# Performance work log

Measured on AMD Instinct MI355X. Metric: run time of the kernel, lower is better.

The kernel has to match this reference:

```python
import jax, jax.numpy as jnp
import numpy as np

NF4_LUT = jnp.array([-1.0, -0.6961928009986877, -0.5250730514526367, -0.39491719007492065,
                     -0.28444138169288635, -0.18477343022823334, -0.08820830285549164, 0.0,
                     0.07107656449079514, 0.14263366162776947, 0.22430233657360077,
                     0.3203405737876892, 0.4407068192958832, 0.5905631184577942,
                     0.796090841293335, 1.0], dtype=jnp.float32)

BLOCK_SIZE = 64
OUT_FEATURES = 11008
IN_FEATURES = 4096


def dequantize_nf4(packed, absmax, out_shape):
    # packed: (O, I//2) int codes 0..255; absmax: (O, num_blocks)
    higher = packed // 16
    lower = packed % 16
    unpacked = jnp.stack([lower, higher], axis=-1).reshape(out_shape)  # (O, I)
    dequant = NF4_LUT[unpacked]  # LUT gather -> fp32 (O, I)
    O, I = out_shape
    # block-wise absmax scale
    dequant = (dequant.reshape(O, I // BLOCK_SIZE, BLOCK_SIZE) * absmax[:, :, None]).reshape(O, I)
    return dequant


def setup_inputs() -> dict:
    key = jax.random.key(0)
    k1, k2, k3, k4 = jax.random.split(key, 4)
    x = jax.random.normal(k1, (4, 2048, IN_FEATURES), dtype=jnp.float32)
    weight = jax.random.randint(k2, (OUT_FEATURES, IN_FEATURES // 2), 0, 256, dtype=jnp.int32)
    absmax = jax.random.uniform(k3, (OUT_FEATURES, IN_FEATURES // BLOCK_SIZE), dtype=jnp.float32)
    bias = jax.random.normal(k4, (OUT_FEATURES,), dtype=jnp.float32)
    return {"x": x, "weight": weight, "absmax": absmax, "bias": bias}


def reference(x, weight, absmax, bias):
    w = dequantize_nf4(weight, absmax, (OUT_FEATURES, IN_FEATURES))  # (O, I)
    # F.linear: y = x @ w.T + bias
    return jnp.einsum('bsi,oi->bso', x, w) + bias
```

## Files before the change

### kernel.cpp

```cpp
#include <hip/hip_runtime.h>

#define IN_F 4096
#define OUT_F 11008

typedef __attribute__((ext_vector_type(8))) short bf16x8;
typedef __attribute__((ext_vector_type(4))) float f32x4;
typedef __attribute__((ext_vector_type(4))) unsigned short us4;
typedef __attribute__((ext_vector_type(8))) unsigned short us8;

__device__ __forceinline__ unsigned short f2bf(float f) {
  unsigned int u = __float_as_uint(f);
  u += 0x7FFFu + ((u >> 16) & 1u);
  return (unsigned short)(u >> 16);
}

__global__ __launch_bounds__(256) void prepass(const float* __restrict__ X,
                                               unsigned short* __restrict__ Xb, int n8,
                                               const int* __restrict__ Wp,
                                               const float* __restrict__ Amax,
                                               unsigned short* __restrict__ Wb, int n4,
                                               int xblk) {
  __shared__ float lutS[16];
  if (threadIdx.x < 16) {
    const float lut[16] = {-1.0f, -0.6961928009986877f, -0.5250730514526367f,
        -0.39491719007492065f, -0.28444138169288635f, -0.18477343022823334f,
        -0.08820830285549164f, 0.0f, 0.07107656449079514f, 0.14263366162776947f,
        0.22430233657360077f, 0.3203405737876892f, 0.4407068192958832f,
        0.5905631184577942f, 0.796090841293335f, 1.0f};
    lutS[threadIdx.x] = lut[threadIdx.x];
  }
  __syncthreads();
  if ((int)blockIdx.x < xblk) {
    for (int i = blockIdx.x * blockDim.x + threadIdx.x; i < n8;
         i += xblk * blockDim.x) {
      const float4 a = reinterpret_cast<const float4*>(X)[2 * i];
      const float4 b = reinterpret_cast<const float4*>(X)[2 * i + 1];
      us8 h;
      h[0] = f2bf(a.x); h[1] = f2bf(a.y); h[2] = f2bf(a.z); h[3] = f2bf(a.w);
      h[4] = f2bf(b.x); h[5] = f2bf(b.y); h[6] = f2bf(b.z); h[7] = f2bf(b.w);
      reinterpret_cast<us8*>(Xb)[i] = h;
    }
  } else {
    const int wgrid = gridDim.x - xblk;
    for (int i = (blockIdx.x - xblk) * blockDim.x + threadIdx.x; i < n4;
         i += wgrid * blockDim.x) {
      const int j = i * 4;
      const int row = j >> 11;
      const int coli = j & 2047;
      const float am = Amax[row * (IN_F / 64) + (coli >> 5)];
      const int4 pk = reinterpret_cast<const int4*>(Wp)[i];
      us8 h; int c;
      c = pk.x & 255; h[0] = f2bf(lutS[c & 15] * am); h[1] = f2bf(lutS[c >> 4] * am);
      c = pk.y & 255; h[2] = f2bf(lutS[c & 15] * am); h[3] = f2bf(lutS[c >> 4] * am);
      c = pk.z & 255; h[4] = f2bf(lutS[c & 15] * am); h[5] = f2bf(lutS[c >> 4] * am);
      c = pk.w & 255; h[6] = f2bf(lutS[c & 15] * am); h[7] = f2bf(lutS[c >> 4] * am);
      reinterpret_cast<us8*>(Wb)[i] = h;
    }
  }
}

#define MF(a, b, c) __builtin_amdgcn_mfma_f32_16x16x32_bf16(a, b, c, 0, 0, 0)
#define GLDS(src, dst) __builtin_amdgcn_global_load_lds( \
    (const __attribute__((address_space(1))) void*)(src), \
    (__attribute__((address_space(3))) void*)(dst), 16, 0, 0)
#define BAR __builtin_amdgcn_s_barrier()
#define VM2 asm volatile("s_waitcnt vmcnt(2)")
#define VM0 asm volatile("s_waitcnt vmcnt(0)")
#define P1 __builtin_amdgcn_s_setprio(1)
#define P0 __builtin_amdgcn_s_setprio(0)

__global__ __launch_bounds__(1024, 4) void gemm256w16(
    const unsigned short* __restrict__ A,
    const unsigned short* __restrict__ B,
    const float* __restrict__ Bias, float* __restrict__ Out, int M) {
  extern __shared__ unsigned short sm[];
  char* const smc = (char*)sm;

  const int tid = threadIdx.x;
  const int l = tid & 63;
  const int wid = tid >> 6;

  const int Nb = OUT_F / 256;

  const int bps = 16 * Nb;
  const int pxc = bps >> 3;
  const int i6 = (int)blockIdx.x % bps;
  const int sup = (int)blockIdx.x / bps;
  const int kk = (i6 & 7) * pxc + (i6 >> 3);
  const int m0 = (sup * 16 + (kk & 15)) * 256;
  const int n0 = (kk >> 4) * 256;

  const int wm = (wid >> 2) * 64;
  const int wn = (wid & 3) * 64;

  const int lv = (l & 15) * 64 + (((l >> 4) ^ ((l >> 1) & 3)) * 16);
  const int aLane = (wid >> 2) * 4096 + lv;
  const int bLane = 16384 + (wid & 3) * 4096 + lv;

  const int rq = tid >> 2;
  const int cs = (tid & 3) ^ ((tid >> 3) & 3);
  const unsigned short* gAs = A + (size_t)(m0 + rq) * IN_F + cs * 8;
  const unsigned short* gBs = B + (size_t)(n0 + rq) * IN_F + cs * 8;

#define SA(t, sl) GLDS(gAs + (size_t)(t) * 32, sm + (sl) * 16384 + wid * 512)
#define SB(t, sl) GLDS(gBs + (size_t)(t) * 32, sm + (sl) * 16384 + 8192 + wid * 512)

  f32x4 acc[4][4];
#pragma unroll
  for (int i = 0; i < 4; ++i)
#pragma unroll
    for (int j = 0; j < 4; ++j) acc[i][j] = {0.f, 0.f, 0.f, 0.f};

#define KT(T, SL, STG, VMW) do { \
    VMW; \
    BAR; \
    const char* Sb = smc + (SL) * 32768; \
    bf16x8 a0, a1, a2, a3, b0, b1, b2, b3; \
    a0 = *(const bf16x8*)(Sb + aLane);        a1 = *(const bf16x8*)(Sb + aLane + 1024); \
    a2 = *(const bf16x8*)(Sb + aLane + 2048); a3 = *(const bf16x8*)(Sb + aLane + 3072); \
    b0 = *(const bf16x8*)(Sb + bLane);        b1 = *(const bf16x8*)(Sb + bLane + 1024); \
    if (STG) SA((T) + 2, ((SL) + 2) % 3); \
    P1; \
    acc[0][0]=MF(a0,b0,acc[0][0]); acc[0][1]=MF(a0,b1,acc[0][1]); \
    acc[1][0]=MF(a1,b0,acc[1][0]); acc[1][1]=MF(a1,b1,acc[1][1]); \
    acc[2][0]=MF(a2,b0,acc[2][0]); acc[2][1]=MF(a2,b1,acc[2][1]); \
    acc[3][0]=MF(a3,b0,acc[3][0]); acc[3][1]=MF(a3,b1,acc[3][1]); \
    P0; \
    b2 = *(const bf16x8*)(Sb + bLane + 2048); b3 = *(const bf16x8*)(Sb + bLane + 3072); \
    if (STG) SB((T) + 2, ((SL) + 2) % 3); \
    P1; \
    acc[0][2]=MF(a0,b2,acc[0][2]); acc[0][3]=MF(a0,b3,acc[0][3]); \
    acc[1][2]=MF(a1,b2,acc[1][2]); acc[1][3]=MF(a1,b3,acc[1][3]); \
    acc[2][2]=MF(a2,b2,acc[2][2]); acc[2][3]=MF(a2,b3,acc[2][3]); \
    acc[3][2]=MF(a3,b2,acc[3][2]); acc[3][3]=MF(a3,b3,acc[3][3]); \
    P0; \
  } while (0)

  SA(0, 0); SB(0, 0); SA(1, 1); SB(1, 1);

  for (int T = 0; T < 126; T += 3) {
    KT(T, 0, (T < 124), VM2);
    KT(T + 1, 1, (T + 1 < 126), VM2);
    KT(T + 2, 2, (T + 2 < 126), VM2);
  }
  KT(126, 0, 0, VM2);
  KT(127, 1, 0, VM0);

  const int crow0 = m0 + wm + ((l >> 4) << 2);
  const int ccol0 = n0 + wn + (l & 15);
#pragma unroll
  for (int j = 0; j < 4; ++j) {
    const float bv = Bias[ccol0 + j * 16];
#pragma unroll
    for (int i = 0; i < 4; ++i)
#pragma unroll
      for (int rg = 0; rg < 4; ++rg)
        Out[(size_t)(crow0 + i * 16 + rg) * OUT_F + ccol0 + j * 16] = acc[i][j][rg] + bv;
  }
}

__global__ __launch_bounds__(256, 2) void nf4_gemm_fused(
    const float* __restrict__ X, const int* __restrict__ Wp,
    const float* __restrict__ Amax, const float* __restrict__ Bias,
    float* __restrict__ Out, int M) {
  __shared__ unsigned short As[128 * 64];
  __shared__ unsigned short Bs[128 * 64];
  __shared__ float lutS[16];

  const int t = threadIdx.x;
  const int l = t & 63;
  const int wid = t >> 6;

  if (t < 16) {
    const float lut[16] = {-1.0f, -0.6961928009986877f, -0.5250730514526367f,
        -0.39491719007492065f, -0.28444138169288635f, -0.18477343022823334f,
        -0.08820830285549164f, 0.0f, 0.07107656449079514f, 0.14263366162776947f,
        0.22430233657360077f, 0.3203405737876892f, 0.4407068192958832f,
        0.5905631184577942f, 0.796090841293335f, 1.0f};
    lutS[t] = lut[t];
  }

  const int ntile = OUT_F / 128;
  const int m0 = (blockIdx.x / ntile) * 128;
  const int n0 = (blockIdx.x % ntile) * 128;

  const int ar = t >> 4;
  const int ac4 = t & 15;
  const int br = t >> 3;
  const int bg = t & 7;
  const int wm = (wid >> 1) * 64;
  const int wn = (wid & 1) * 64;

  f32x4 acc[4][4];
#pragma unroll
  for (int i = 0; i < 4; ++i)
#pragma unroll
    for (int j = 0; j < 4; ++j) acc[i][j] = {0.f, 0.f, 0.f, 0.f};

  __syncthreads();

  for (int k0 = 0; k0 < IN_F; k0 += 64) {
#pragma unroll
    for (int p = 0; p < 8; ++p) {
      const int r = p * 16 + ar;
      const float4 v = *reinterpret_cast<const float4*>(
          X + (size_t)(m0 + r) * IN_F + k0 + ac4 * 4);
      us4 h;
      h[0] = f2bf(v.x); h[1] = f2bf(v.y); h[2] = f2bf(v.z); h[3] = f2bf(v.w);
      const int byte = r * 128 + ((ac4 * 8) ^ ((r & 7) << 4));
      *reinterpret_cast<us4*>(reinterpret_cast<char*>(As) + byte) = h;
    }
#pragma unroll
    for (int p = 0; p < 4; ++p) {
      const int r = p * 32 + br;
      const float amv = Amax[(size_t)(n0 + r) * (IN_F / 64) + (k0 >> 6)];
      const int4 pk = *reinterpret_cast<const int4*>(
          Wp + (size_t)(n0 + r) * (IN_F / 2) + (k0 >> 1) + bg * 4);
      us8 h;
      {
        int c;
        c = pk.x & 255; h[0] = f2bf(lutS[c & 15] * amv); h[1] = f2bf(lutS[c >> 4] * amv);
        c = pk.y & 255; h[2] = f2bf(lutS[c & 15] * amv); h[3] = f2bf(lutS[c >> 4] * amv);
        c = pk.z & 255; h[4] = f2bf(lutS[c & 15] * amv); h[5] = f2bf(lutS[c >> 4] * amv);
        c = pk.w & 255; h[6] = f2bf(lutS[c & 15] * amv); h[7] = f2bf(lutS[c >> 4] * amv);
      }
      const int byte = r * 128 + ((bg * 16) ^ ((r & 7) << 4));
      *reinterpret_cast<us8*>(reinterpret_cast<char*>(Bs) + byte) = h;
    }
    __syncthreads();

#pragma unroll
    for (int kkk = 0; kkk < 64; kkk += 32) {
      bf16x8 af[4], bfv[4];
      const int kb = (kkk + ((l >> 4) << 3)) * 2;
#pragma unroll
      for (int i = 0; i < 4; ++i) {
        const int row = wm + i * 16 + (l & 15);
        af[i] = *reinterpret_cast<const bf16x8*>(
            reinterpret_cast<const char*>(As) + row * 128 + (kb ^ ((row & 7) << 4)));
      }
#pragma unroll
      for (int j = 0; j < 4; ++j) {
        const int row = wn + j * 16 + (l & 15);
        bfv[j] = *reinterpret_cast<const bf16x8*>(
            reinterpret_cast<const char*>(Bs) + row * 128 + (kb ^ ((row & 7) << 4)));
      }
#pragma unroll
      for (int i = 0; i < 4; ++i)
#pragma unroll
        for (int j = 0; j < 4; ++j)
          acc[i][j] = __builtin_amdgcn_mfma_f32_16x16x32_bf16(af[i], bfv[j], acc[i][j], 0, 0, 0);
    }
    __syncthreads();
  }

  const int crow0 = m0 + wm + ((l >> 4) << 2);
  const int ccol0 = n0 + wn + (l & 15);
#pragma unroll
  for (int j = 0; j < 4; ++j) {
    const float bv = Bias[ccol0 + j * 16];
#pragma unroll
    for (int i = 0; i < 4; ++i)
#pragma unroll
      for (int rg = 0; rg < 4; ++rg)
        Out[(size_t)(crow0 + i * 16 + rg) * OUT_F + ccol0 + j * 16] = acc[i][j][rg] + bv;
  }
}

extern "C" void kernel_launch(void* const* d_in, const int* in_sizes, int n_in,
                              void* d_out, int out_size, void* d_ws, size_t ws_size,
                              hipStream_t stream) {
  const float* X = (const float*)d_in[0];
  const int* Wp = (const int*)d_in[1];
  const float* Amax = (const float*)d_in[2];
  const float* Bias = (const float*)d_in[3];
  float* Out = (float*)d_out;

  const int M = in_sizes[0] / IN_F;
  const size_t needX = (size_t)M * IN_F * 2;
  const size_t needW = (size_t)OUT_F * IN_F * 2;
  const int grid256 = (M / 256) * (OUT_F / 256);

  if (ws_size >= needX + needW && (M % 4096) == 0) {
    unsigned short* Xb = (unsigned short*)d_ws;
    unsigned short* Wb = Xb + (size_t)M * IN_F;
    (void)hipFuncSetAttribute(reinterpret_cast<const void*>(gemm256w16),
                              hipFuncAttributeMaxDynamicSharedMemorySize, 98304);
    prepass<<<4096, 256, 0, stream>>>(X, Xb, M * (IN_F / 8),
                                      Wp, Amax, Wb, OUT_F * (IN_F / 8), 2048);
    gemm256w16<<<grid256, 1024, 98304, stream>>>(Xb, Wb, Bias, Out, M);
  } else {
    const int grid = (M / 128) * (OUT_F / 128);
    nf4_gemm_fused<<<grid, 256, 0, stream>>>(X, Wp, Amax, Bias, Out, M);
  }
}
```

Baseline: 752.5 us.

## Halve GEMM block to 8 waves with 128x64 warp tiles and register double-buffering

The 256x256 bf16 GEMM now runs with 512 threads (8 waves) instead of 1024. Each wave computes a 128x64 sub-tile (8x4 MFMA accumulators) and each thread issues two global-to-LDS loads per operand per k-step. LDS fragments for the next k-tile are read into a second register set while MFMAs run on the current one, so LDS reads overlap the math. The wait changes to vmcnt(0) every iteration. Register pressure roughly doubles and there are fewer waves to hide latency, which could reduce occupancy or cause spills.

```diff
diff --git a/kernel.cpp b/kernel.cpp
--- a/kernel.cpp
+++ b/kernel.cpp
@@ -64,12 +64,12 @@
     (const __attribute__((address_space(1))) void*)(src), \
     (__attribute__((address_space(3))) void*)(dst), 16, 0, 0)
 #define BAR __builtin_amdgcn_s_barrier()
-#define VM2 asm volatile("s_waitcnt vmcnt(2)")
+#define VM4 asm volatile("s_waitcnt vmcnt(4)")
 #define VM0 asm volatile("s_waitcnt vmcnt(0)")
 #define P1 __builtin_amdgcn_s_setprio(1)
 #define P0 __builtin_amdgcn_s_setprio(0)
 
-__global__ __launch_bounds__(1024, 4) void gemm256w16(
+__global__ __launch_bounds__(512, 2) void gemm256p(
     const unsigned short* __restrict__ A,
     const unsigned short* __restrict__ B,
     const float* __restrict__ Bias, float* __restrict__ Out, int M) {
@@ -90,69 +90,100 @@
   const int m0 = (sup * 16 + (kk & 15)) * 256;
   const int n0 = (kk >> 4) * 256;
 
-  const int wm = (wid >> 2) * 64;
-  const int wn = (wid & 3) * 64;
+  const int wmw = (wid >> 2);
+  const int wnw = (wid & 3);
 
   const int lv = (l & 15) * 64 + (((l >> 4) ^ ((l >> 1) & 3)) * 16);
-  const int aLane = (wid >> 2) * 4096 + lv;
-  const int bLane = 16384 + (wid & 3) * 4096 + lv;
+  const int aLane = wmw * 8192 + lv;
+  const int bLane = 16384 + wnw * 4096 + lv;
 
   const int rq = tid >> 2;
   const int cs = (tid & 3) ^ ((tid >> 3) & 3);
   const unsigned short* gAs = A + (size_t)(m0 + rq) * IN_F + cs * 8;
   const unsigned short* gBs = B + (size_t)(n0 + rq) * IN_F + cs * 8;
 
-#define SA(t, sl) GLDS(gAs + (size_t)(t) * 32, sm + (sl) * 16384 + wid * 512)
-#define SB(t, sl) GLDS(gBs + (size_t)(t) * 32, sm + (sl) * 16384 + 8192 + wid * 512)
-
-  f32x4 acc[4][4];
-#pragma unroll
-  for (int i = 0; i < 4; ++i)
+#define SA(t, sl) do { \
+    unsigned short* d_ = sm + (sl) * 16384 + wid * 512; \
+    const unsigned short* s_ = gAs + (size_t)(t) * 32; \
+    GLDS(s_, d_); GLDS(s_ + (size_t)128 * IN_F, d_ + 4096); } while (0)
+#define SB(t, sl) do { \
+    unsigned short* d_ = sm + (sl) * 16384 + 8192 + wid * 512; \
+    const unsigned short* s_ = gBs + (size_t)(t) * 32; \
+    GLDS(s_, d_); GLDS(s_ + (size_t)128 * IN_F, d_ + 4096); } while (0)
+
+  bf16x8 xa0, xa1, xa2, xa3, xa4, xa5, xa6, xa7, xb0, xb1, xb2, xb3;
+  bf16x8 ya0, ya1, ya2, ya3, ya4, ya5, ya6, ya7, yb0, yb1, yb2, yb3;
+
+#define RD12(PX, SL) do { const char* Rb = smc + (SL) * 32768; \
+    PX##a0 = *(const bf16x8*)(Rb + aLane);        PX##a1 = *(const bf16x8*)(Rb + aLane + 1024); \
+    PX##a2 = *(const bf16x8*)(Rb + aLane + 2048); PX##a3 = *(const bf16x8*)(Rb + aLane + 3072); \
+    PX##a4 = *(const bf16x8*)(Rb + aLane + 4096); PX##a5 = *(const bf16x8*)(Rb + aLane + 5120); \
+    PX##a6 = *(const bf16x8*)(Rb + aLane + 6144); PX##a7 = *(const bf16x8*)(Rb + aLane + 7168); \
+    PX##b0 = *(const bf16x8*)(Rb + bLane);        PX##b1 = *(const bf16x8*)(Rb + bLane + 1024); \
+    PX##b2 = *(const bf16x8*)(Rb + bLane + 2048); PX##b3 = *(const bf16x8*)(Rb + bLane + 3072); \
+  } while (0)
+
+  f32x4 acc[8][4];
+#pragma unroll
+  for (int i = 0; i < 8; ++i)
 #pragma unroll
     for (int j = 0; j < 4; ++j) acc[i][j] = {0.f, 0.f, 0.f, 0.f};
 
-#define KT(T, SL, STG, VMW) do { \
-    VMW; \
+#define MM16LO(PX) do { P1; \
+    acc[0][0]=MF(PX##a0,PX##b0,acc[0][0]); acc[0][1]=MF(PX##a0,PX##b1,acc[0][1]); \
+    acc[0][2]=MF(PX##a0,PX##b2,acc[0][2]); acc[0][3]=MF(PX##a0,PX##b3,acc[0][3]); \
+    acc[1][0]=MF(PX##a1,PX##b0,acc[1][0]); acc[1][1]=MF(PX##a1,PX##b1,acc[1][1]); \
+    acc[1][2]=MF(PX##a1,PX##b2,acc[1][2]); acc[1][3]=MF(PX##a1,PX##b3,acc[1][3]); \
+    acc[2][0]=MF(PX##a2,PX##b0,acc[2][0]); acc[2][1]=MF(PX##a2,PX##b1,acc[2][1]); \
+    acc[2][2]=MF(PX##a2,PX##b2,acc[2][2]); acc[2][3]=MF(PX##a2,PX##b3,acc[2][3]); \
+    acc[3][0]=MF(PX##a3,PX##b0,acc[3][0]); acc[3][1]=MF(PX##a3,PX##b1,acc[3][1]); \
+    acc[3][2]=MF(PX##a3,PX##b2,acc[3][2]); acc[3][3]=MF(PX##a3,PX##b3,acc[3][3]); \
+    P0; } while (0)
+#define MM16HI(PX) do { P1; \
+    acc[4][0]=MF(PX##a4,PX##b0,acc[4][0]); acc[4][1]=MF(PX##a4,PX##b1,acc[4][1]); \
+    acc[4][2]=MF(PX##a4,PX##b2,acc[4][2]); acc[4][3]=MF(PX##a4,PX##b3,acc[4][3]); \
+    acc[5][0]=MF(PX##a5,PX##b0,acc[5][0]); acc[5][1]=MF(PX##a5,PX##b1,acc[5][1]); \
+    acc[5][2]=MF(PX##a5,PX##b2,acc[5][2]); acc[5][3]=MF(PX##a5,PX##b3,acc[5][3]); \
+    acc[6][0]=MF(PX##a6,PX##b0,acc[6][0]); acc[6][1]=MF(PX##a6,PX##b1,acc[6][1]); \
+    acc[6][2]=MF(PX##a6,PX##b2,acc[6][2]); acc[6][3]=MF(PX##a6,PX##b3,acc[6][3]); \
+    acc[7][0]=MF(PX##a7,PX##b0,acc[7][0]); acc[7][1]=MF(PX##a7,PX##b1,acc[7][1]); \
+    acc[7][2]=MF(PX##a7,PX##b2,acc[7][2]); acc[7][3]=MF(PX##a7,PX##b3,acc[7][3]); \
+    P0; } while (0)
+
+#define KT(T, SLRD, SLST, STG, MMSET, RDSET) do { \
+    VM0; \
     BAR; \
-    const char* Sb = smc + (SL) * 32768; \
-    bf16x8 a0, a1, a2, a3, b0, b1, b2, b3; \
-    a0 = *(const bf16x8*)(Sb + aLane);        a1 = *(const bf16x8*)(Sb + aLane + 1024); \
-    a2 = *(const bf16x8*)(Sb + aLane + 2048); a3 = *(const bf16x8*)(Sb + aLane + 3072); \
-    b0 = *(const bf16x8*)(Sb + bLane);        b1 = *(const bf16x8*)(Sb + bLane + 1024); \
-    if (STG) SA((T) + 2, ((SL) + 2) % 3); \
-    P1; \
-    acc[0][0]=MF(a0,b0,acc[0][0]); acc[0][1]=MF(a0,b1,acc[0][1]); \
-    acc[1][0]=MF(a1,b0,acc[1][0]); acc[1][1]=MF(a1,b1,acc[1][1]); \
-    acc[2][0]=MF(a2,b0,acc[2][0]); acc[2][1]=MF(a2,b1,acc[2][1]); \
-    acc[3][0]=MF(a3,b0,acc[3][0]); acc[3][1]=MF(a3,b1,acc[3][1]); \
-    P0; \
-    b2 = *(const bf16x8*)(Sb + bLane + 2048); b3 = *(const bf16x8*)(Sb + bLane + 3072); \
-    if (STG) SB((T) + 2, ((SL) + 2) % 3); \
-    P1; \
-    acc[0][2]=MF(a0,b2,acc[0][2]); acc[0][3]=MF(a0,b3,acc[0][3]); \
-    acc[1][2]=MF(a1,b2,acc[1][2]); acc[1][3]=MF(a1,b3,acc[1][3]); \
-    acc[2][2]=MF(a2,b2,acc[2][2]); acc[2][3]=MF(a2,b3,acc[2][3]); \
-    acc[3][2]=MF(a3,b2,acc[3][2]); acc[3][3]=MF(a3,b3,acc[3][3]); \
-    P0; \
+    RD12(RDSET, SLRD); \
+    if (STG) SA((T) + 2, SLST); \
+    MM16LO(MMSET); \
+    if (STG) SB((T) + 2, SLST); \
+    MM16HI(MMSET); \
   } while (0)
 
   SA(0, 0); SB(0, 0); SA(1, 1); SB(1, 1);
-
-  for (int T = 0; T < 126; T += 3) {
-    KT(T, 0, (T < 124), VM2);
-    KT(T + 1, 1, (T + 1 < 126), VM2);
-    KT(T + 2, 2, (T + 2 < 126), VM2);
-  }
-  KT(126, 0, 0, VM2);
-  KT(127, 1, 0, VM0);
-
-  const int crow0 = m0 + wm + ((l >> 4) << 2);
-  const int ccol0 = n0 + wn + (l & 15);
+  VM4;
+  BAR;
+  RD12(x, 0);
+
+  for (int T = 0; T < 126; T += 6) {
+    KT(T + 0, 1, 2, 1, x, y);
+    KT(T + 1, 2, 0, 1, y, x);
+    KT(T + 2, 0, 1, 1, x, y);
+    KT(T + 3, 1, 2, 1, y, x);
+    KT(T + 4, 2, 0, 1, x, y);
+    KT(T + 5, 0, 1, 1, y, x);
+  }
+  KT(126, 1, 0, 0, x, y);
+  MM16LO(y);
+  MM16HI(y);
+
+  const int crow0 = m0 + wmw * 128 + ((l >> 4) << 2);
+  const int ccol0 = n0 + wnw * 64 + (l & 15);
 #pragma unroll
   for (int j = 0; j < 4; ++j) {
     const float bv = Bias[ccol0 + j * 16];
 #pragma unroll
-    for (int i = 0; i < 4; ++i)
+    for (int i = 0; i < 8; ++i)
 #pragma unroll
       for (int rg = 0; rg < 4; ++rg)
         Out[(size_t)(crow0 + i * 16 + rg) * OUT_F + ccol0 + j * 16] = acc[i][j][rg] + bv;
@@ -284,11 +315,11 @@
   if (ws_size >= needX + needW && (M % 4096) == 0) {
     unsigned short* Xb = (unsigned short*)d_ws;
     unsigned short* Wb = Xb + (size_t)M * IN_F;
-    (void)hipFuncSetAttribute(reinterpret_cast<const void*>(gemm256w16),
+    (void)hipFuncSetAttribute(reinterpret_cast<const void*>(gemm256p),
                               hipFuncAttributeMaxDynamicSharedMemorySize, 98304);
     prepass<<<4096, 256, 0, stream>>>(X, Xb, M * (IN_F / 8),
                                       Wp, Amax, Wb, OUT_F * (IN_F / 8), 2048);
-    gemm256w16<<<grid256, 1024, 98304, stream>>>(Xb, Wb, Bias, Out, M);
+    gemm256p<<<grid256, 512, 98304, stream>>>(Xb, Wb, Bias, Out, M);
   } else {
     const int grid = (M / 128) * (OUT_F / 128);
     nf4_gemm_fused<<<grid, 256, 0, stream>>>(X, Wp, Amax, Bias, Out, M);
```

New measurement: 888.5 us. +18.1%, slower.
